# Kernel optimization log

Measured on AMD Instinct MI355X. Metric: run time of the kernel, lower is better.

Reference implementation:

```python
import jax, jax.numpy as jnp
import numpy as np
from jax import lax

B = 8192      # image batch
S = 32        # seq_length
I = 16        # ltc_input_size (sensory neurons)
U = 19        # ltc_hidden_size (units)
M = 2         # num_classes (motor neurons)
UNFOLDS = 6   # ncps LTCCell default ode_unfolds
EPS = 1e-8


def setup_inputs() -> dict:
    key = jax.random.key(0)
    ks = jax.random.split(key, 24)
    u = lambda k, sh, lo, hi: jax.random.uniform(k, sh, jnp.float32, lo, hi)
    x = jax.random.normal(ks[0], (B, 1, 28, 44), jnp.float32)
    conv1_w = jax.random.normal(ks[1], (6, 1, 5, 5), jnp.float32) * 0.2
    conv1_b = u(ks[2], (6,), -0.1, 0.1)
    conv2_w = jax.random.normal(ks[3], (16, 6, 5, 5), jnp.float32) * 0.08
    conv2_b = u(ks[4], (16,), -0.1, 0.1)
    # wiring adjacency (AutoNCP approximated by random sparse +/-1 polarity)
    sparsity_mask = (jax.random.uniform(ks[5], (U, U)) < 0.5).astype(jnp.float32)
    sensory_sparsity_mask = (jax.random.uniform(ks[6], (I, U)) < 0.5).astype(jnp.float32)
    erev = sparsity_mask * jnp.where(jax.random.uniform(ks[7], (U, U)) < 0.8, 1.0, -1.0)
    sensory_erev = sensory_sparsity_mask * jnp.where(jax.random.uniform(ks[8], (I, U)) < 0.8, 1.0, -1.0)
    # LTCCell parameter init ranges from ncps
    gleak = u(ks[9], (U,), 0.001, 1.0)
    vleak = u(ks[10], (U,), -0.2, 0.2)
    cm = u(ks[11], (U,), 0.4, 0.6)
    sigma = u(ks[12], (U, U), 3.0, 8.0)
    mu = u(ks[13], (U, U), 0.3, 0.8)
    w = u(ks[14], (U, U), 0.001, 1.0)
    sensory_sigma = u(ks[15], (I, U), 3.0, 8.0)
    sensory_mu = u(ks[16], (I, U), 0.3, 0.8)
    sensory_w = u(ks[17], (I, U), 0.001, 1.0)
    input_w = jnp.ones((I,), jnp.float32)
    input_b = jnp.zeros((I,), jnp.float32)
    output_w = jnp.ones((M,), jnp.float32)
    output_b = jnp.zeros((M,), jnp.float32)
    return dict(x=x, conv1_w=conv1_w, conv1_b=conv1_b, conv2_w=conv2_w, conv2_b=conv2_b,
                gleak=gleak, vleak=vleak, cm=cm, sigma=sigma, mu=mu, w=w, erev=erev,
                sensory_sigma=sensory_sigma, sensory_mu=sensory_mu, sensory_w=sensory_w,
                sensory_erev=sensory_erev, input_w=input_w, input_b=input_b,
                output_w=output_w, output_b=output_b,
                sparsity_mask=sparsity_mask, sensory_sparsity_mask=sensory_sparsity_mask)


def _maxpool2(h):
    return lax.reduce_window(h, -jnp.inf, lax.max, (1, 1, 2, 2), (1, 1, 2, 2), 'VALID')


def reference(x, conv1_w, conv1_b, conv2_w, conv2_b, gleak, vleak, cm, sigma, mu, w,
              erev, sensory_sigma, sensory_mu, sensory_w, sensory_erev, input_w, input_b,
              output_w, output_b, sparsity_mask, sensory_sparsity_mask):
    dn = ('NCHW', 'OIHW', 'NCHW')
    h = lax.conv_general_dilated(x, conv1_w, (1, 1), 'VALID', dimension_numbers=dn)
    h = _maxpool2(jax.nn.relu(h + conv1_b[None, :, None, None]))
    h = lax.conv_general_dilated(h, conv2_w, (1, 1), 'VALID', dimension_numbers=dn)
    h = _maxpool2(jax.nn.relu(h + conv2_b[None, :, None, None]))
    feat = h.reshape(h.shape[0], -1).reshape(-1, S, I)   # (B, 32, 16)
    seq = jnp.swapaxes(feat, 0, 1)                       # (S, B, I)
    cm_t = cm * UNFOLDS                                  # cm / (elapsed_time/unfolds), dt=1

    def step(v, inp):
        inp = inp * input_w + input_b                    # sensory affine mapping
        # sensory synapse activations (B, I, U), fixed over the ODE unfolds
        s_act = sensory_w * jax.nn.sigmoid(sensory_sigma * (inp[:, :, None] - sensory_mu))
        s_act = s_act * sensory_sparsity_mask
        w_num_s = jnp.sum(s_act * sensory_erev, axis=1)
        w_den_s = jnp.sum(s_act, axis=1)

        def unfold(vv, _):
            wa = w * jax.nn.sigmoid(sigma * (vv[:, :, None] - mu)) * sparsity_mask  # (B,U,U)
            num = cm_t * vv + gleak * vleak + jnp.sum(wa * erev, axis=1) + w_num_s
            den = cm_t + gleak + jnp.sum(wa, axis=1) + w_den_s
            return num / (den + EPS), None

        v, _ = lax.scan(unfold, v, None, length=UNFOLDS)
        return v, None

    v0 = jnp.zeros((feat.shape[0], U), x.dtype)
    vT, _ = lax.scan(step, v0, seq)
    # motor mapping: first M neurons, affine output map; equals out[:, -1, :]
    return vT[:, :M] * output_w + output_b
```

## Files before the change

kernel.cpp:

```cpp
#include <hip/hip_runtime.h>

#define BTOT 8192
#define SEQ 32
#define IPB 6
#define TPB 128
#define L2E 1.4426950408889634f
#define FSTRIDE 520
#define LSTRIDE 528
#define RSL 16

__global__ void prep_w2t(const float* __restrict__ w2, float* __restrict__ wt) {
    int idx = blockIdx.x * blockDim.x + threadIdx.x;
    if (idx < 2400) {
        int k = idx >> 4, c2 = idx & 15;
        wt[idx] = w2[c2 * 150 + k];
    }
}

__global__ __launch_bounds__(128, 4) void conv_k(
    const float* __restrict__ xin,
    const float* __restrict__ w1, const float* __restrict__ b1,
    const float* __restrict__ b2, const float* __restrict__ wt,
    float* __restrict__ featG)
{
    __shared__ __align__(16) float img[1232];
    __shared__ __align__(16) float c1p[1440];
    const int tid = threadIdx.x;
    const int bG = blockIdx.x;

    for (int idx = tid; idx < 1232; idx += 128) img[idx] = xin[bG * 1232 + idx];
    __syncthreads();
    for (int idx = tid; idx < 240; idx += 128) {
        int y = idx / 20, xx = idx - (idx / 20) * 20;
        const float* ib = img + (2 * y) * 44 + 2 * xx;
        float win[6][6];
        #pragma unroll
        for (int r = 0; r < 6; ++r) {
            float2 a = *(const float2*)(ib + r * 44);
            float2 b = *(const float2*)(ib + r * 44 + 2);
            float2 c = *(const float2*)(ib + r * 44 + 4);
            win[r][0] = a.x; win[r][1] = a.y; win[r][2] = b.x;
            win[r][3] = b.y; win[r][4] = c.x; win[r][5] = c.y;
        }
        for (int ch = 0; ch < 6; ++ch) {
            const float* wp = w1 + ch * 25;
            float a00 = 0.f, a01 = 0.f, a10 = 0.f, a11 = 0.f;
            #pragma unroll
            for (int ky = 0; ky < 5; ++ky)
                #pragma unroll
                for (int kx = 0; kx < 5; ++kx) {
                    float wv = wp[ky * 5 + kx];
                    a00 = fmaf(wv, win[ky][kx], a00);
                    a01 = fmaf(wv, win[ky][kx + 1], a01);
                    a10 = fmaf(wv, win[ky + 1][kx], a10);
                    a11 = fmaf(wv, win[ky + 1][kx + 1], a11);
                }
        float m = fmaxf(fmaxf(a00, a01), fmaxf(a10, a11)) + b1[ch];
            c1p[ch * 240 + idx] = fmaxf(m, 0.f);
        }
    }
    __syncthreads();
    {
        const int oy = tid >> 4, ox = tid & 15;
        float acc[16];
        #pragma unroll
        for (int c2 = 0; c2 < 16; ++c2) acc[c2] = 0.f;
        for (int ch = 0; ch < 6; ++ch) {
            const float* rowb = c1p + ch * 240 + oy * 20 + ox;
            const float* wch = wt + (ch * 25 << 4);
            #pragma unroll
            for (int ky = 0; ky < 5; ++ky) {
                #pragma unroll
                for (int kx = 0; kx < 5; ++kx) {
                    float xv = rowb[ky * 20 + kx];
                    const float4* wk = (const float4*)(wch + ((ky * 5 + kx) << 4));
                    float4 wa = wk[0], wb = wk[1], wc = wk[2], wd = wk[3];
                    acc[0]  = fmaf(wa.x, xv, acc[0]);  acc[1]  = fmaf(wa.y, xv, acc[1]);
                    acc[2]  = fmaf(wa.z, xv, acc[2]);  acc[3]  = fmaf(wa.w, xv, acc[3]);
                    acc[4]  = fmaf(wb.x, xv, acc[4]);  acc[5]  = fmaf(wb.y, xv, acc[5]);
                    acc[6]  = fmaf(wb.z, xv, acc[6]);  acc[7]  = fmaf(wb.w, xv, acc[7]);
                    acc[8]  = fmaf(wc.x, xv, acc[8]);  acc[9]  = fmaf(wc.y, xv, acc[9]);
                    acc[10] = fmaf(wc.z, xv, acc[10]); acc[11] = fmaf(wc.w, xv, acc[11]);
                    acc[12] = fmaf(wd.x, xv, acc[12]); acc[13] = fmaf(wd.y, xv, acc[13]);
                    acc[14] = fmaf(wd.z, xv, acc[14]); acc[15] = fmaf(wd.w, xv, acc[15]);
                }
            }
        }
        const bool wl = ((tid & 1) == 0) && ((tid & 16) == 0);
        const int obase = (oy >> 1) * 8 + (ox >> 1);
        #pragma unroll
        for (int c2 = 0; c2 < 16; ++c2) {
            float a = acc[c2];
            a = fmaxf(a, __shfl_xor(a, 1));
            a = fmaxf(a, __shfl_xor(a, 16));
            if (wl) img[obase + c2 * 32] = fmaxf(a + b2[c2], 0.f);
        }
    }
    __syncthreads();
    if (tid < 128) ((float4*)(featG + bG * 512))[tid] = ((const float4*)img)[tid];
}

__global__ __launch_bounds__(64, 4) void ltc_k(
    const float* __restrict__ featG,
    const float* __restrict__ gleak, const float* __restrict__ vleak, const float* __restrict__ cm,
    const float* __restrict__ sigma, const float* __restrict__ mu, const float* __restrict__ ww,
    const float* __restrict__ erev,
    const float* __restrict__ ssigma, const float* __restrict__ smu, const float* __restrict__ sw,
    const float* __restrict__ serev,
    const float* __restrict__ inw, const float* __restrict__ inb,
    const float* __restrict__ outw, const float* __restrict__ outb,
    const float* __restrict__ mask, const float* __restrict__ smask,
    float* __restrict__ dout)
{
    __shared__ __align__(16) float pp[2736];
    __shared__ __align__(16) float featL[3 * LSTRIDE];
    __shared__ int ncol[19], mcol[19], cnts[2];
    float2* rAB = (float2*)pp;
    float2* rZI = (float2*)(pp + 760);
    float2* sAB = (float2*)(pp + 1520);
    float2* sZI = (float2*)(pp + 2128);

    const int tid = threadIdx.x;
    const int b0 = blockIdx.x * 3;

    for (int idx = tid; idx < 384; idx += 64) {
        int k = idx >> 7, r = idx & 127;
        float4 val = {0.f, 0.f, 0.f, 0.f};
        if (b0 + k < BTOT) val = ((const float4*)(featG + (b0 + k) * 512))[r];
        *(float4*)(featL + k * LSTRIDE + r * 4) = val;
    }
    for (int idx = tid; idx < 2736; idx += 64) pp[idx] = 0.f;
    __syncthreads();
    if (tid < 19) {
        const int jj = tid;
        int c = 0;
        for (int i = 0; i < 19; ++i) {
            int idx = i * 19 + jj;
            if (mask[idx] != 0.f) {
                float s = sigma[idx];
                rAB[c * 19 + jj] = make_float2(-L2E * s, L2E * s * mu[idx]);
                rZI[c * 19 + jj] = make_float2(ww[idx] * erev[idx], __int_as_float(i));
                ++c;
            }
        }
        ncol[jj] = c;
        c = 0;
        for (int i = 0; i < 16; ++i) {
            int idx = i * 19 + jj;
            if (smask[idx] != 0.f) {
                float s = ssigma[idx];
                sAB[c * 19 + jj] = make_float2(-L2E * s * inw[i],
                                               -L2E * s * (inb[i] - smu[idx]));
                sZI[c * 19 + jj] = make_float2(sw[idx] * serev[idx], __int_as_float(i));
                ++c;
            }
        }
        mcol[jj] = c;
    }
    __syncthreads();
    if (tid == 0) {
        int MRv = 0, MSv = 0;
        for (int j2 = 0; j2 < 19; ++j2) {
            MRv = max(MRv, ncol[j2]);
            MSv = max(MSv, mcol[j2]);
        }
        cnts[0] = MRv;
        cnts[1] = MSv;
    }
    __syncthreads();
    const int MR = __builtin_amdgcn_readfirstlane(cnts[0]);
    const int MS = __builtin_amdgcn_readfirstlane(cnts[1]);

    const int l = tid;
    const int g = l / 19;
    const int j = l - g * 19;
    const int gbase = g * 19;
    const int kimg = (g < 3) ? g : 2;
    const bool act = (g < 3) && (b0 + g < BTOT);

    float UA[RSL], UB[RSL], UZ[RSL];
    int LI[RSL];
    #pragma unroll
    for (int c = 0; c < RSL; ++c) {
        float2 ab = rAB[c * 19 + j];
        float2 zi = rZI[c * 19 + j];
        UA[c] = ab.x; UB[c] = ab.y; UZ[c] = zi.x;
        LI[c] = gbase + __float_as_int(zi.y);
    }
    #pragma unroll
    for (int c = 0; c < RSL; ++c)
        asm volatile("" : "+v"(UA[c]), "+v"(UB[c]), "+v"(UZ[c]), "+v"(LI[c]));

    const float gl = gleak[j];
    const float gv = gl * vleak[j];
    const float cmt = cm[j] * 6.f;

    float v = 0.f;
    const float* frow = featL + kimg * LSTRIDE;

    #pragma unroll 1
    for (int st = 0; st < SEQ; ++st) {
        const float* fb = frow + st * 16;
        float wn0 = 0.f, wn1 = 0.f, wd0 = 0.f, wd1 = 0.f;
        #pragma unroll 1
        for (int c = 0; c + 1 < MS; c += 2) {
            float2 ab0 = sAB[c * 19 + j],        zi0 = sZI[c * 19 + j];
            float2 ab1 = sAB[(c + 1) * 19 + j],  zi1 = sZI[(c + 1) * 19 + j];
            float t0 = fmaf(ab0.x, fb[__float_as_int(zi0.y)], ab0.y);
            float t1 = fmaf(ab1.x, fb[__float_as_int(zi1.y)], ab1.y);
            float r0 = __builtin_amdgcn_rcpf(1.f + __builtin_amdgcn_exp2f(t0));
            float r1 = __builtin_amdgcn_rcpf(1.f + __builtin_amdgcn_exp2f(t1));
            wn0 = fmaf(zi0.x, r0, wn0); wd0 = fmaf(fabsf(zi0.x), r0, wd0);
            wn1 = fmaf(zi1.x, r1, wn1); wd1 = fmaf(fabsf(zi1.x), r1, wd1);
        }
        if (MS & 1) {
            int c = MS - 1;
            float2 ab = sAB[c * 19 + j], zi = sZI[c * 19 + j];
            float t = fmaf(ab.x, fb[__float_as_int(zi.y)], ab.y);
            float r = __builtin_amdgcn_rcpf(1.f + __builtin_amdgcn_exp2f(t));
            wn0 = fmaf(zi.x, r, wn0); wd0 = fmaf(fabsf(zi.x), r, wd0);
        }
        const float nb = gv + (wn0 + wn1);
        const float db = cmt + gl + (wd0 + wd1);
        #pragma unroll 1
        for (int u = 0; u < 6; ++u) {
            float n0 = fmaf(cmt, v, nb), n1 = 0.f, n2 = 0.f, n3 = 0.f;
            float d0 = db, d1 = 0.f, d2 = 0.f, d3 = 0.f;
            #pragma unroll
            for (int c = 0; c < RSL; c += 4) {
                float v0 = __shfl(v, LI[c]);
                float v1 = __shfl(v, LI[c + 1]);
                float v2 = __shfl(v, LI[c + 2]);
                float v3 = __shfl(v, LI[c + 3]);
                float t0 = fmaf(UA[c], v0, UB[c]);
                float t1 = fmaf(UA[c + 1], v1, UB[c + 1]);
                float t2 = fmaf(UA[c + 2], v2, UB[c + 2]);
                float t3 = fmaf(UA[c + 3], v3, UB[c + 3]);
                float r0 = __builtin_amdgcn_rcpf(1.f + __builtin_amdgcn_exp2f(t0));
                float r1 = __builtin_amdgcn_rcpf(1.f + __builtin_amdgcn_exp2f(t1));
                float r2 = __builtin_amdgcn_rcpf(1.f + __builtin_amdgcn_exp2f(t2));
                float r3 = __builtin_amdgcn_rcpf(1.f + __builtin_amdgcn_exp2f(t3));
                n0 = fmaf(UZ[c], r0, n0);     d0 = fmaf(fabsf(UZ[c]), r0, d0);
                n1 = fmaf(UZ[c + 1], r1, n1); d1 = fmaf(fabsf(UZ[c + 1]), r1, d1);
                n2 = fmaf(UZ[c + 2], r2, n2); d2 = fmaf(fabsf(UZ[c + 2]), r2, d2);
                n3 = fmaf(UZ[c + 3], r3, n3); d3 = fmaf(fabsf(UZ[c + 3]), r3, d3);
            }
            float num = (n0 + n1) + (n2 + n3);
            float den = (d0 + d1) + (d2 + d3);
            #pragma unroll 1
            for (int c = RSL; c < MR; ++c) {
                float2 ab = rAB[c * 19 + j], zi = rZI[c * 19 + j];
                float vv = __shfl(v, gbase + __float_as_int(zi.y));
                float t = fmaf(ab.x, vv, ab.y);
                float r = __builtin_amdgcn_rcpf(1.f + __builtin_amdgcn_exp2f(t));
                num = fmaf(zi.x, r, num);
                den = fmaf(fabsf(zi.x), r, den);
            }
            v = num * __builtin_amdgcn_rcpf(den + 1e-8f);
        }
    }
    if (act && j < 2) dout[(b0 + g) * 2 + j] = fmaf(v, outw[j], outb[j]);
}

__global__ __launch_bounds__(TPB, 3) void ltc_fused(
    const float* __restrict__ xin,
    const float* __restrict__ w1, const float* __restrict__ b1,
    const float* __restrict__ b2,
    const float* __restrict__ gleak, const float* __restrict__ vleak, const float* __restrict__ cm,
    const float* __restrict__ sigma, const float* __restrict__ mu, const float* __restrict__ ww,
    const float* __restrict__ erev,
    const float* __restrict__ ssigma, const float* __restrict__ smu, const float* __restrict__ sw,
    const float* __restrict__ serev,
    const float* __restrict__ inw, const float* __restrict__ inb,
    const float* __restrict__ outw, const float* __restrict__ outb,
    const float* __restrict__ mask, const float* __restrict__ smask,
    const float* __restrict__ wt,
    float* __restrict__ dout)
{
    __shared__ __align__(16) float uni[2736];
    __shared__ __align__(16) float featL[IPB * FSTRIDE];
    __shared__ int ncol[19], mcol[19], cnts[2];

    float* img = uni;
    float* c1p = uni + 1232;
    float2* rAB = (float2*)uni;
    float2* rZI = (float2*)(uni + 760);
    float2* sAB = (float2*)(uni + 1520);
    float2* sZI = (float2*)(uni + 2128);

    const int tid = threadIdx.x;
    const int b0 = blockIdx.x * IPB;

    for (int k = 0; k < IPB; ++k) {
        const int bG = b0 + k;
        const bool valid = bG < BTOT;
        if (valid) {
            for (int idx = tid; idx < 1232; idx += TPB) img[idx] = xin[bG * 1232 + idx];
        }
        __syncthreads();
        if (valid) {
            for (int idx = tid; idx < 240; idx += TPB) {
                int y = idx / 20, xx = idx - (idx / 20) * 20;
                const float* ib = img + (2 * y) * 44 + 2 * xx;
                float win[6][6];
                #pragma unroll
                for (int r = 0; r < 6; ++r) {
                    float2 a = *(const float2*)(ib + r * 44);
                    float2 b = *(const float2*)(ib + r * 44 + 2);
                    float2 c = *(const float2*)(ib + r * 44 + 4);
                    win[r][0] = a.x; win[r][1] = a.y; win[r][2] = b.x;
                    win[r][3] = b.y; win[r][4] = c.x; win[r][5] = c.y;
                }
                for (int ch = 0; ch < 6; ++ch) {
                    const float* wp = w1 + ch * 25;
                    float a00 = 0.f, a01 = 0.f, a10 = 0.f, a11 = 0.f;
                    #pragma unroll
                    for (int ky = 0; ky < 5; ++ky)
                        #pragma unroll
                        for (int kx = 0; kx < 5; ++kx) {
                            float wv = wp[ky * 5 + kx];
                            a00 = fmaf(wv, win[ky][kx], a00);
                            a01 = fmaf(wv, win[ky][kx + 1], a01);
                            a10 = fmaf(wv, win[ky + 1][kx], a10);
                            a11 = fmaf(wv, win[ky + 1][kx + 1], a11);
                        }
                    float m = fmaxf(fmaxf(a00, a01), fmaxf(a10, a11)) + b1[ch];
                    c1p[ch * 240 + idx] = fmaxf(m, 0.f);
                }
            }
        }
        __syncthreads();
        if (valid) {
            const int oy = tid >> 4, ox = tid & 15;
            float acc[16];
            #pragma unroll
            for (int c2 = 0; c2 < 16; ++c2) acc[c2] = 0.f;
            for (int ch = 0; ch < 6; ++ch) {
                const float* rowb = c1p + ch * 240 + oy * 20 + ox;
                const float* wch = wt + (ch * 25 << 4);
                #pragma unroll
                for (int ky = 0; ky < 5; ++ky) {
                    #pragma unroll
                    for (int kx = 0; kx < 5; ++kx) {
                        float xv = rowb[ky * 20 + kx];
                        const float4* wk = (const float4*)(wch + ((ky * 5 + kx) << 4));
                        float4 wa = wk[0], wb = wk[1], wc = wk[2], wd = wk[3];
                        acc[0]  = fmaf(wa.x, xv, acc[0]);  acc[1]  = fmaf(wa.y, xv, acc[1]);
                        acc[2]  = fmaf(wa.z, xv, acc[2]);  acc[3]  = fmaf(wa.w, xv, acc[3]);
                        acc[4]  = fmaf(wb.x, xv, acc[4]);  acc[5]  = fmaf(wb.y, xv, acc[5]);
                        acc[6]  = fmaf(wb.z, xv, acc[6]);  acc[7]  = fmaf(wb.w, xv, acc[7]);
                        acc[8]  = fmaf(wc.x, xv, acc[8]);  acc[9]  = fmaf(wc.y, xv, acc[9]);
                        acc[10] = fmaf(wc.z, xv, acc[10]); acc[11] = fmaf(wc.w, xv, acc[11]);
                        acc[12] = fmaf(wd.x, xv, acc[12]); acc[13] = fmaf(wd.y, xv, acc[13]);
                        acc[14] = fmaf(wd.z, xv, acc[14]); acc[15] = fmaf(wd.w, xv, acc[15]);
                    }
                }
            }
            const bool wl = ((tid & 1) == 0) && ((tid & 16) == 0);
            const int obase = k * FSTRIDE + (oy >> 1) * 8 + (ox >> 1);
            #pragma unroll
            for (int c2 = 0; c2 < 16; ++c2) {
                float a = acc[c2];
                a = fmaxf(a, __shfl_xor(a, 1));
                a = fmaxf(a, __shfl_xor(a, 16));
                if (wl) featL[obase + c2 * 32] = fmaxf(a + b2[c2], 0.f);
            }
        }
        __syncthreads();
    }

    for (int idx = tid; idx < 2736; idx += TPB) uni[idx] = 0.f;
    __syncthreads();
    if (tid < 19) {
        const int jj = tid;
        int c = 0;
        for (int i = 0; i < 19; ++i) {
            int idx = i * 19 + jj;
            if (mask[idx] != 0.f) {
                float s = sigma[idx];
                rAB[c * 19 + jj] = make_float2(-L2E * s, L2E * s * mu[idx]);
                rZI[c * 19 + jj] = make_float2(ww[idx] * erev[idx], __int_as_float(i));
                ++c;
            }
        }
        ncol[jj] = c;
        c = 0;
        for (int i = 0; i < 16; ++i) {
            int idx = i * 19 + jj;
            if (smask[idx] != 0.f) {
                float s = ssigma[idx];
                sAB[c * 19 + jj] = make_float2(-L2E * s * inw[i],
                                               -L2E * s * (inb[i] - smu[idx]));
                sZI[c * 19 + jj] = make_float2(sw[idx] * serev[idx], __int_as_float(i));
                ++c;
            }
        }
        mcol[jj] = c;
    }
    __syncthreads();
    if (tid == 0) {
        int MRv = 0, MSv = 0;
        for (int j2 = 0; j2 < 19; ++j2) {
            MRv = max(MRv, ncol[j2]);
            MSv = max(MSv, mcol[j2]);
        }
        cnts[0] = MRv;
        cnts[1] = MSv;
    }
    __syncthreads();
    const int MR = __builtin_amdgcn_readfirstlane(cnts[0]);
    const int MS = __builtin_amdgcn_readfirstlane(cnts[1]);

    const int wv_ = tid >> 6, l = tid & 63;
    const int g = l / 19;
    const int j = l - g * 19;
    const int gbase = g * 19;
    const int kimg = wv_ * 3 + g;
    const bool act = (g < 3) && (b0 + kimg < BTOT);
    const int kc = (kimg < IPB) ? kimg : (IPB - 1);

    float UA[RSL], UB[RSL], UZ[RSL];
    int LI[RSL];
    #pragma unroll
    for (int c = 0; c < RSL; ++c) {
        float2 ab = rAB[c * 19 + j];
        float2 zi = rZI[c * 19 + j];
        UA[c] = ab.x; UB[c] = ab.y; UZ[c] = zi.x;
        LI[c] = gbase + __float_as_int(zi.y);
    }
    #pragma unroll
    for (int c = 0; c < RSL; ++c)
        asm volatile("" : "+v"(UA[c]), "+v"(UB[c]), "+v"(UZ[c]), "+v"(LI[c]));

    const float gl = gleak[j];
    const float gv = gl * vleak[j];
    const float cmt = cm[j] * 6.f;

    float v = 0.f;
    const float* frow = featL + kc * FSTRIDE;

    #pragma unroll 1
    for (int st = 0; st < SEQ; ++st) {
        const float* fb = frow + st * 16;
        float wns = 0.f, wds = 0.f;
        #pragma unroll 1
        for (int c = 0; c < MS; ++c) {
            float2 ab = sAB[c * 19 + j];
            float2 zi = sZI[c * 19 + j];
            float f = fb[__float_as_int(zi.y)];
            float t = fmaf(ab.x, f, ab.y);
            float r = __builtin_amdgcn_rcpf(1.f + __builtin_amdgcn_exp2f(t));
            wns = fmaf(zi.x, r, wns);
            wds = fmaf(fabsf(zi.x), r, wds);
        }
        const float nb = gv + wns;
        const float db = cmt + gl + wds;
        #pragma unroll 1
        for (int u = 0; u < 6; ++u) {
            float num = fmaf(cmt, v, nb);
            float den = db;
            #pragma unroll
            for (int c = 0; c < RSL; ++c) {
                float vv = __shfl(v, LI[c]);
                float t = fmaf(UA[c], vv, UB[c]);
                float r = __builtin_amdgcn_rcpf(1.f + __builtin_amdgcn_exp2f(t));
                num = fmaf(UZ[c], r, num);
                den = fmaf(fabsf(UZ[c]), r, den);
            }
            #pragma unroll 1
            for (int c = RSL; c < MR; ++c) {
                float2 ab = rAB[c * 19 + j];
                float2 zi = rZI[c * 19 + j];
                float vv = __shfl(v, gbase + __float_as_int(zi.y));
                float t = fmaf(ab.x, vv, ab.y);
                float r = __builtin_amdgcn_rcpf(1.f + __builtin_amdgcn_exp2f(t));
                num = fmaf(zi.x, r, num);
                den = fmaf(fabsf(zi.x), r, den);
            }
            v = num * __builtin_amdgcn_rcpf(den + 1e-8f);
        }
    }
    if (act && j < 2) dout[(b0 + kimg) * 2 + j] = fmaf(v, outw[j], outb[j]);
}

extern "C" void kernel_launch(void* const* d_in, const int* in_sizes, int n_in,
                              void* d_out, int out_size, void* d_ws, size_t ws_size,
                              hipStream_t stream) {
    const float* x      = (const float*)d_in[0];
    const float* w1     = (const float*)d_in[1];
    const float* b1     = (const float*)d_in[2];
    const float* w2     = (const float*)d_in[3];
    const float* b2     = (const float*)d_in[4];
    const float* gleak  = (const float*)d_in[5];
    const float* vleak  = (const float*)d_in[6];
    const float* cm     = (const float*)d_in[7];
    const float* sigma  = (const float*)d_in[8];
    const float* mu     = (const float*)d_in[9];
    const float* ww     = (const float*)d_in[10];
    const float* erev   = (const float*)d_in[11];
    const float* ssig   = (const float*)d_in[12];
    const float* smu    = (const float*)d_in[13];
    const float* sw     = (const float*)d_in[14];
    const float* serev  = (const float*)d_in[15];
    const float* inw    = (const float*)d_in[16];
    const float* inb    = (const float*)d_in[17];
    const float* outw   = (const float*)d_in[18];
    const float* outb   = (const float*)d_in[19];
    const float* mask   = (const float*)d_in[20];
    const float* smask  = (const float*)d_in[21];

    float* wt = (float*)d_ws;
    float* featG = (float*)d_ws + 4096;
    const size_t need = (size_t)4096 * 4 + (size_t)BTOT * 512 * 4;

    hipLaunchKernelGGL(prep_w2t, dim3(10), dim3(256), 0, stream, w2, wt);

    if (ws_size >= need) {
        hipLaunchKernelGGL(conv_k, dim3(BTOT), dim3(128), 0, stream,
                           x, w1, b1, b2, (const float*)wt, featG);
        hipLaunchKernelGGL(ltc_k, dim3((BTOT + 2) / 3), dim3(64), 0, stream,
                           (const float*)featG, gleak, vleak, cm, sigma, mu, ww, erev,
                           ssig, smu, sw, serev, inw, inb, outw, outb, mask, smask,
                           (float*)d_out);
    } else {
        hipLaunchKernelGGL(ltc_fused, dim3((BTOT + IPB - 1) / IPB), dim3(TPB), 0, stream,
                           x, w1, b1, b2, gleak, vleak, cm, sigma, mu, ww, erev,
                           ssig, smu, sw, serev, inw, inb, outw, outb, mask, smask,
                           (const float*)wt, (float*)d_out);
    }
}
```

Baseline: 369.9 us.

## Precompute sensory synapse sums in conv kernel and hoist parameter packing to prep kernel

Moves the compressed-sparse parameter packing out of every ltc_k block into a one-shot prep_params kernel whose output lives in workspace. The sensory-synapse weighted sums (wn, wd) for each image, timestep and unit are now computed in the conv kernel, which has 128 threads per image, and written to global memory. The serial ltc_k recurrence then only reads one float2 per step, prefetched one step ahead. The ODE unfold inner loop also drops from four partial accumulators to two. The cost is a larger intermediate buffer (8192×32×19 float2, about 40 MB against the 16 MB feature buffer it replaces), more work inside conv_k, and possible changes in occupancy or ILP.

```diff
diff --git a/kernel.cpp b/kernel.cpp
--- a/kernel.cpp
+++ b/kernel.cpp
@@ -6,8 +6,8 @@
 #define TPB 128
 #define L2E 1.4426950408889634f
 #define FSTRIDE 520
-#define LSTRIDE 528
 #define RSL 16
+
 
 __global__ void prep_w2t(const float* __restrict__ w2, float* __restrict__ wt) {
     int idx = blockIdx.x * blockDim.x + threadIdx.x;
@@ -17,11 +17,71 @@
     }
 }
 
+__global__ void prep_params(
+    const float* __restrict__ sigma, const float* __restrict__ mu,
+    const float* __restrict__ ww, const float* __restrict__ erev,
+    const float* __restrict__ ssigma, const float* __restrict__ smu,
+    const float* __restrict__ sw, const float* __restrict__ serev,
+    const float* __restrict__ inw, const float* __restrict__ inb,
+    const float* __restrict__ mask, const float* __restrict__ smask,
+    float* __restrict__ ws)
+{
+    __shared__ int ncol[19], mcol[19];
+    float2* rAB = (float2*)(ws + 4096);
+    float2* rZI = (float2*)(ws + 4864);
+    float2* sAB = (float2*)(ws + 5632);
+    float2* sZI = (float2*)(ws + 6240);
+    int* cnt = (int*)(ws + 6848);
+    const int j = threadIdx.x;
+    if (j < 19) {
+        for (int c = 0; c < 19; ++c) {
+            rAB[c * 19 + j] = make_float2(0.f, 0.f);
+            rZI[c * 19 + j] = make_float2(0.f, __int_as_float(0));
+        }
+        for (int c = 0; c < 16; ++c) {
+            sAB[c * 19 + j] = make_float2(0.f, 0.f);
+            sZI[c * 19 + j] = make_float2(0.f, __int_as_float(0));
+        }
+        int c = 0;
+        for (int i = 0; i < 19; ++i) {
+            int idx = i * 19 + j;
+            if (mask[idx] != 0.f) {
+                float s = sigma[idx];
+                rAB[c * 19 + j] = make_float2(-L2E * s, L2E * s * mu[idx]);
+                rZI[c * 19 + j] = make_float2(ww[idx] * erev[idx], __int_as_float(i));
+                ++c;
+            }
+        }
+        ncol[j] = c;
+        c = 0;
+        for (int i = 0; i < 16; ++i) {
+            int idx = i * 19 + j;
+            if (smask[idx] != 0.f) {
+                float s = ssigma[idx];
+                sAB[c * 19 + j] = make_float2(-L2E * s * inw[i],
+                                              -L2E * s * (inb[i] - smu[idx]));
+                sZI[c * 19 + j] = make_float2(sw[idx] * serev[idx], __int_as_float(i));
+                ++c;
+            }
+        }
+        mcol[j] = c;
+    }
+    __syncthreads();
+    if (j == 0) {
+        int MR = 0, MS = 0;
+        for (int k = 0; k < 19; ++k) { MR = max(MR, ncol[k]); MS = max(MS, mcol[k]); }
+        cnt[0] = MR;
+        cnt[1] = MS;
+    }
+}
+
 __global__ __launch_bounds__(128, 4) void conv_k(
     const float* __restrict__ xin,
     const float* __restrict__ w1, const float* __restrict__ b1,
     const float* __restrict__ b2, const float* __restrict__ wt,
-    float* __restrict__ featG)
+    const float* __restrict__ sparam,
+    const int* __restrict__ cnt,
+    float2* __restrict__ wnwd)
 {
     __shared__ __align__(16) float img[1232];
     __shared__ __align__(16) float c1p[1440];
@@ -55,7 +115,7 @@
                     a10 = fmaf(wv, win[ky + 1][kx], a10);
                     a11 = fmaf(wv, win[ky + 1][kx + 1], a11);
                 }
-        float m = fmaxf(fmaxf(a00, a01), fmaxf(a10, a11)) + b1[ch];
+            float m = fmaxf(fmaxf(a00, a01), fmaxf(a10, a11)) + b1[ch];
             c1p[ch * 240 + idx] = fmaxf(m, 0.f);
         }
     }
@@ -97,86 +157,48 @@
         }
     }
     __syncthreads();
-    if (tid < 128) ((float4*)(featG + bG * 512))[tid] = ((const float4*)img)[tid];
+    for (int idx = tid; idx < 1216; idx += 128) c1p[idx] = sparam[idx];
+    __syncthreads();
+    {
+        const float2* sAB2 = (const float2*)c1p;
+        const float2* sZI2 = (const float2*)(c1p + 608);
+        const float* featI = img;
+        const int MS = cnt[1];
+        for (int p = tid; p < 608; p += 128) {
+            int st = p / 19, j = p - (p / 19) * 19;
+            float wn = 0.f, wd = 0.f;
+            for (int c = 0; c < MS; ++c) {
+                float2 ab = sAB2[c * 19 + j];
+                float2 zi = sZI2[c * 19 + j];
+                float f = featI[st * 16 + __float_as_int(zi.y)];
+                float t = fmaf(ab.x, f, ab.y);
+                float r = __builtin_amdgcn_rcpf(1.f + __builtin_amdgcn_exp2f(t));
+                wn = fmaf(zi.x, r, wn);
+                wd = fmaf(fabsf(zi.x), r, wd);
+            }
+            wnwd[(bG * SEQ + st) * 19 + j] = make_float2(wn, wd);
+        }
+    }
 }
 
-__global__ __launch_bounds__(64, 4) void ltc_k(
-    const float* __restrict__ featG,
-    const float* __restrict__ gleak, const float* __restrict__ vleak, const float* __restrict__ cm,
-    const float* __restrict__ sigma, const float* __restrict__ mu, const float* __restrict__ ww,
-    const float* __restrict__ erev,
-    const float* __restrict__ ssigma, const float* __restrict__ smu, const float* __restrict__ sw,
-    const float* __restrict__ serev,
-    const float* __restrict__ inw, const float* __restrict__ inb,
+__global__ __launch_bounds__(64, 3) void ltc_k(
+    const float2* __restrict__ wnwd,
+    const float* __restrict__ rABg_, const float* __restrict__ rZIg_,
+    const int* __restrict__ cnt,
+    const float* __restrict__ gleak, const float* __restrict__ vleak,
+    const float* __restrict__ cm,
     const float* __restrict__ outw, const float* __restrict__ outb,
-    const float* __restrict__ mask, const float* __restrict__ smask,
     float* __restrict__ dout)
 {
-    __shared__ __align__(16) float pp[2736];
-    __shared__ __align__(16) float featL[3 * LSTRIDE];
-    __shared__ int ncol[19], mcol[19], cnts[2];
-    float2* rAB = (float2*)pp;
-    float2* rZI = (float2*)(pp + 760);
-    float2* sAB = (float2*)(pp + 1520);
-    float2* sZI = (float2*)(pp + 2128);
-
-    const int tid = threadIdx.x;
-    const int b0 = blockIdx.x * 3;
-
-    for (int idx = tid; idx < 384; idx += 64) {
-        int k = idx >> 7, r = idx & 127;
-        float4 val = {0.f, 0.f, 0.f, 0.f};
-        if (b0 + k < BTOT) val = ((const float4*)(featG + (b0 + k) * 512))[r];
-        *(float4*)(featL + k * LSTRIDE + r * 4) = val;
-    }
-    for (int idx = tid; idx < 2736; idx += 64) pp[idx] = 0.f;
-    __syncthreads();
-    if (tid < 19) {
-        const int jj = tid;
-        int c = 0;
-        for (int i = 0; i < 19; ++i) {
-            int idx = i * 19 + jj;
-            if (mask[idx] != 0.f) {
-                float s = sigma[idx];
-                rAB[c * 19 + jj] = make_float2(-L2E * s, L2E * s * mu[idx]);
-                rZI[c * 19 + jj] = make_float2(ww[idx] * erev[idx], __int_as_float(i));
-                ++c;
-            }
-        }
-        ncol[jj] = c;
-        c = 0;
-        for (int i = 0; i < 16; ++i) {
-            int idx = i * 19 + jj;
-            if (smask[idx] != 0.f) {
-                float s = ssigma[idx];
-                sAB[c * 19 + jj] = make_float2(-L2E * s * inw[i],
-                                               -L2E * s * (inb[i] - smu[idx]));
-                sZI[c * 19 + jj] = make_float2(sw[idx] * serev[idx], __int_as_float(i));
-                ++c;
-            }
-        }
-        mcol[jj] = c;
-    }
-    __syncthreads();
-    if (tid == 0) {
-        int MRv = 0, MSv = 0;
-        for (int j2 = 0; j2 < 19; ++j2) {
-            MRv = max(MRv, ncol[j2]);
-            MSv = max(MSv, mcol[j2]);
-        }
-        cnts[0] = MRv;
-        cnts[1] = MSv;
-    }
-    __syncthreads();
-    const int MR = __builtin_amdgcn_readfirstlane(cnts[0]);
-    const int MS = __builtin_amdgcn_readfirstlane(cnts[1]);
-
-    const int l = tid;
+    const float2* rAB = (const float2*)rABg_;
+    const float2* rZI = (const float2*)rZIg_;
+    const int l = threadIdx.x;
     const int g = l / 19;
     const int j = l - g * 19;
     const int gbase = g * 19;
-    const int kimg = (g < 3) ? g : 2;
+    const int b0 = blockIdx.x * 3;
     const bool act = (g < 3) && (b0 + g < BTOT);
+    const int img = min(b0 + ((g < 3) ? g : 2), BTOT - 1);
 
     float UA[RSL], UB[RSL], UZ[RSL];
     int LI[RSL];
@@ -191,65 +213,38 @@
     for (int c = 0; c < RSL; ++c)
         asm volatile("" : "+v"(UA[c]), "+v"(UB[c]), "+v"(UZ[c]), "+v"(LI[c]));
 
+    const int MR = cnt[0];
     const float gl = gleak[j];
     const float gv = gl * vleak[j];
     const float cmt = cm[j] * 6.f;
 
     float v = 0.f;
-    const float* frow = featL + kimg * LSTRIDE;
+    const float2* wrow = wnwd + img * SEQ * 19 + j;
+    float2 wcur = wrow[0];
 
     #pragma unroll 1
     for (int st = 0; st < SEQ; ++st) {
-        const float* fb = frow + st * 16;
-        float wn0 = 0.f, wn1 = 0.f, wd0 = 0.f, wd1 = 0.f;
-        #pragma unroll 1
-        for (int c = 0; c + 1 < MS; c += 2) {
-            float2 ab0 = sAB[c * 19 + j],        zi0 = sZI[c * 19 + j];
-            float2 ab1 = sAB[(c + 1) * 19 + j],  zi1 = sZI[(c + 1) * 19 + j];
-            float t0 = fmaf(ab0.x, fb[__float_as_int(zi0.y)], ab0.y);
-            float t1 = fmaf(ab1.x, fb[__float_as_int(zi1.y)], ab1.y);
-            float r0 = __builtin_amdgcn_rcpf(1.f + __builtin_amdgcn_exp2f(t0));
-            float r1 = __builtin_amdgcn_rcpf(1.f + __builtin_amdgcn_exp2f(t1));
-            wn0 = fmaf(zi0.x, r0, wn0); wd0 = fmaf(fabsf(zi0.x), r0, wd0);
-            wn1 = fmaf(zi1.x, r1, wn1); wd1 = fmaf(fabsf(zi1.x), r1, wd1);
-        }
-        if (MS & 1) {
-            int c = MS - 1;
-            float2 ab = sAB[c * 19 + j], zi = sZI[c * 19 + j];
-            float t = fmaf(ab.x, fb[__float_as_int(zi.y)], ab.y);
-            float r = __builtin_amdgcn_rcpf(1.f + __builtin_amdgcn_exp2f(t));
-            wn0 = fmaf(zi.x, r, wn0); wd0 = fmaf(fabsf(zi.x), r, wd0);
-        }
-        const float nb = gv + (wn0 + wn1);
-        const float db = cmt + gl + (wd0 + wd1);
+        float2 wnext = (st < SEQ - 1) ? wrow[(st + 1) * 19] : wcur;
+        const float nb = gv + wcur.x;
+        const float db = cmt + gl + wcur.y;
         #pragma unroll 1
         for (int u = 0; u < 6; ++u) {
-            float n0 = fmaf(cmt, v, nb), n1 = 0.f, n2 = 0.f, n3 = 0.f;
-            float d0 = db, d1 = 0.f, d2 = 0.f, d3 = 0.f;
+            float n0 = fmaf(cmt, v, nb), n1 = 0.f;
+            float d0 = db, d1 = 0.f;
             #pragma unroll
-            for (int c = 0; c < RSL; c += 4) {
-                float v0 = __shfl(v, LI[c]);
-                float v1 = __shfl(v, LI[c + 1]);
-                float v2 = __shfl(v, LI[c + 2]);
-                float v3 = __shfl(v, LI[c + 3]);
-                float t0 = fmaf(UA[c], v0, UB[c]);
-                float t1 = fmaf(UA[c + 1], v1, UB[c + 1]);
-                float t2 = fmaf(UA[c + 2], v2, UB[c + 2]);
-                float t3 = fmaf(UA[c + 3], v3, UB[c + 3]);
-                float r0 = __builtin_amdgcn_rcpf(1.f + __builtin_amdgcn_exp2f(t0));
-                float r1 = __builtin_amdgcn_rcpf(1.f + __builtin_amdgcn_exp2f(t1));
-                float r2 = __builtin_amdgcn_rcpf(1.f + __builtin_amdgcn_exp2f(t2));
-                float r3 = __builtin_amdgcn_rcpf(1.f + __builtin_amdgcn_exp2f(t3));
-                n0 = fmaf(UZ[c], r0, n0);     d0 = fmaf(fabsf(UZ[c]), r0, d0);
-                n1 = fmaf(UZ[c + 1], r1, n1); d1 = fmaf(fabsf(UZ[c + 1]), r1, d1);
-                n2 = fmaf(UZ[c + 2], r2, n2); d2 = fmaf(fabsf(UZ[c + 2]), r2, d2);
-                n3 = fmaf(UZ[c + 3], r3, n3); d3 = fmaf(fabsf(UZ[c + 3]), r3, d3);
-            }
-            float num = (n0 + n1) + (n2 + n3);
-            float den = (d0 + d1) + (d2 + d3);
+            for (int c = 0; c < RSL; ++c) {
+                float vv = __shfl(v, LI[c]);
+                float t = fmaf(UA[c], vv, UB[c]);
+                float r = __builtin_amdgcn_rcpf(1.f + __builtin_amdgcn_exp2f(t));
+                if (c & 1) { n1 = fmaf(UZ[c], r, n1); d1 = fmaf(fabsf(UZ[c]), r, d1); }
+                else       { n0 = fmaf(UZ[c], r, n0); d0 = fmaf(fabsf(UZ[c]), r, d0); }
+            }
+            float num = n0 + n1;
+            float den = d0 + d1;
             #pragma unroll 1
             for (int c = RSL; c < MR; ++c) {
-                float2 ab = rAB[c * 19 + j], zi = rZI[c * 19 + j];
+                float2 ab = rAB[c * 19 + j];
+                float2 zi = rZI[c * 19 + j];
                 float vv = __shfl(v, gbase + __float_as_int(zi.y));
                 float t = fmaf(ab.x, vv, ab.y);
                 float r = __builtin_amdgcn_rcpf(1.f + __builtin_amdgcn_exp2f(t));
@@ -258,6 +253,7 @@
             }
             v = num * __builtin_amdgcn_rcpf(den + 1e-8f);
         }
+        wcur = wnext;
     }
     if (act && j < 2) dout[(b0 + g) * 2 + j] = fmaf(v, outw[j], outb[j]);
 }
@@ -509,23 +505,28 @@
     const float* mask   = (const float*)d_in[20];
     const float* smask  = (const float*)d_in[21];
 
-    float* wt = (float*)d_ws;
-    float* featG = (float*)d_ws + 4096;
-    const size_t need = (size_t)4096 * 4 + (size_t)BTOT * 512 * 4;
-
-    hipLaunchKernelGGL(prep_w2t, dim3(10), dim3(256), 0, stream, w2, wt);
+    float* ws = (float*)d_ws;
+    const size_t need = (size_t)(8192 + (size_t)BTOT * SEQ * 19 * 2) * 4;
+
+    hipLaunchKernelGGL(prep_w2t, dim3(10), dim3(256), 0, stream, w2, ws);
 
     if (ws_size >= need) {
+        hipLaunchKernelGGL(prep_params, dim3(1), dim3(64), 0, stream,
+                           sigma, mu, ww, erev, ssig, smu, sw, serev, inw, inb,
+                           mask, smask, ws);
         hipLaunchKernelGGL(conv_k, dim3(BTOT), dim3(128), 0, stream,
-                           x, w1, b1, b2, (const float*)wt, featG);
+                           x, w1, b1, b2, (const float*)ws,
+                           (const float*)(ws + 5632), (const int*)(ws + 6848),
+                           (float2*)(ws + 8192));
         hipLaunchKernelGGL(ltc_k, dim3((BTOT + 2) / 3), dim3(64), 0, stream,
-                           (const float*)featG, gleak, vleak, cm, sigma, mu, ww, erev,
-                           ssig, smu, sw, serev, inw, inb, outw, outb, mask, smask,
-                           (float*)d_out);
+                           (const float2*)(ws + 8192),
+                           (const float*)(ws + 4096), (const float*)(ws + 4864),
+                           (const int*)(ws + 6848),
+                           gleak, vleak, cm, outw, outb, (float*)d_out);
     } else {
         hipLaunchKernelGGL(ltc_fused, dim3((BTOT + IPB - 1) / IPB), dim3(TPB), 0, stream,
                            x, w1, b1, b2, gleak, vleak, cm, sigma, mu, ww, erev,
                            ssig, smu, sw, serev, inw, inb, outw, outb, mask, smask,
-                           (const float*)wt, (float*)d_out);
+                           (const float*)ws, (float*)d_out);
     }
 }
```

After: 337.9 us. -8.7%, faster.
